# Optimization experiments

Measured on AMD Instinct MI355X. Metric: run time of the kernel, lower is better.

Reference implementation:

```python
import jax, jax.numpy as jnp
import numpy as np

HEADS = 16
DIM_HEAD = 64


def setup_inputs() -> dict:
    key = jax.random.key(0)
    k1, k2, k3, k4 = jax.random.split(key, 4)
    b, sq, skv, dim = 2, 2048, 2048, 1024
    inner = HEADS * DIM_HEAD
    return {
        "x_q": jax.random.normal(k1, (b, sq, dim), dtype=jnp.float32),
        "x_kv": jax.random.normal(k2, (b, skv, dim), dtype=jnp.float32),
        "W_qkv": jax.random.normal(k3, (dim, 3 * inner), dtype=jnp.float32) * (dim ** -0.5),
        "W_out": jax.random.normal(k4, (inner, dim), dtype=jnp.float32) * (inner ** -0.5),
        "b_out": jnp.zeros((dim,), dtype=jnp.float32),
    }


def reference(x_q, x_kv, W_qkv, W_out, b_out):
    b, sq, dim = x_q.shape
    skv = x_kv.shape[1]
    inner = HEADS * DIM_HEAD
    scale = DIM_HEAD ** -0.5
    # to_qkv on concat([x_q, x_kv], seq) as in the original (bias-free linear)
    qkv = jnp.concatenate([x_q, x_kv], axis=1) @ W_qkv  # [b, sq+skv, 3*inner]
    q, k, v = jnp.split(qkv, 3, axis=-1)
    q = q[:, :sq].reshape(b, sq, HEADS, DIM_HEAD).transpose(0, 2, 1, 3)   # [b,h,sq,d]
    k = k[:, sq:].reshape(b, skv, HEADS, DIM_HEAD).transpose(0, 2, 1, 3)  # [b,h,skv,d]
    v = v[:, sq:].reshape(b, skv, HEADS, DIM_HEAD).transpose(0, 2, 1, 3)  # [b,h,skv,d]
    dots = jnp.einsum('bhqd,bhkd->bhqk', q, k) * scale
    attn = jax.nn.softmax(dots, axis=-1)  # dropout p=0.0 -> identity
    out = jnp.einsum('bhqk,bhkd->bhqd', attn, v)
    out = out.transpose(0, 2, 1, 3).reshape(b, sq, inner)
    return out @ W_out + b_out
```

## Files before the change

### kernel.cpp

```cpp
#include <hip/hip_runtime.h>


typedef __attribute__((ext_vector_type(8))) short short8;
typedef __attribute__((ext_vector_type(4))) short short4v;
typedef __attribute__((ext_vector_type(4))) float floatx4;
typedef __attribute__((ext_vector_type(16))) float floatx16;

#define QSCALE 0.18033688f

#if __has_builtin(__builtin_amdgcn_exp2f)
#define EXP2(x) __builtin_amdgcn_exp2f(x)
#else
#define EXP2(x) exp2f(x)
#endif

__device__ __forceinline__ ushort f2b(float f) {
  union { float f; unsigned u; } x; x.f = f;
  unsigned r = (x.u + 0x7fffu + ((x.u >> 16) & 1u)) >> 16;
  return (ushort)r;
}

__device__ __forceinline__ unsigned f2b2(float a, float b) {
  union { float f; unsigned u; } x, y; x.f = a; y.f = b;
  return __builtin_amdgcn_perm(y.u + 0x8000u, x.u + 0x8000u, 0x07060302u);
}

__device__ __forceinline__ unsigned cvtpk(float a, float b) {
  unsigned r;
  asm("v_cvt_pk_bf16_f32 %0, %1, %2" : "=v"(r) : "v"(a), "v"(b));
  return r;
}

#define GLL(gp, lp)                                                            \
  __builtin_amdgcn_global_load_lds(                                            \
      (const __attribute__((address_space(1))) void*)(gp),                     \
      (__attribute__((address_space(3))) void*)(lp), 16, 0, 0)

__global__ void prep(const float* __restrict__ xq, const float* __restrict__ xkv,
                     ushort* __restrict__ oq, ushort* __restrict__ okv,
                     const float* __restrict__ Wqkv, ushort* __restrict__ WqkvT,
                     const float* __restrict__ Wout, ushort* __restrict__ WoutT) {
  __shared__ float tile[32][33];
  int bid = blockIdx.x;
  const int n = 4096 * 1024;
  if (bid < 2048) {
    bool lo = bid < 1024;
    const float* in = lo ? xq : xkv;
    ushort* out = lo ? oq : okv;
    int b2 = lo ? bid : bid - 1024;
    int stride = 1024 * 256 * 4;
    for (int i = (b2 * 256 + (int)threadIdx.x) * 4; i < n; i += stride) {
      float4 v = *(const float4*)(in + i);
      uint2 o;
      o.x = f2b2(v.x, v.y);
      o.y = f2b2(v.z, v.w);
      *(uint2*)(out + i) = o;
    }
    return;
  }
  int tb = bid - 2048;
  int bx = tb & 127, by = tb >> 7;
  bool first = bx < 96;
  const float* in = first ? Wqkv : Wout;
  ushort* out = first ? WqkvT : WoutT;
  int N = first ? 3072 : 1024;
  int bxx = first ? bx : bx - 96;
  int k0 = by * 32, n0 = bxx * 32;
  int tx = threadIdx.x & 31, ty = threadIdx.x >> 5;
#pragma unroll
  for (int i = 0; i < 32; i += 8)
    tile[ty + i][tx] = in[(size_t)(k0 + ty + i) * N + n0 + tx];
  __syncthreads();
#pragma unroll
  for (int i = 0; i < 32; i += 8)
    out[(size_t)(n0 + ty + i) * 1024 + k0 + tx] = f2b(tile[tx][ty + i]);
}

__global__ __launch_bounds__(256, 3) void gemm_qkv(
    const ushort* __restrict__ Aq, const ushort* __restrict__ Akv,
    const ushort* __restrict__ Bt,
    ushort* __restrict__ Cq, ushort* __restrict__ Ck, ushort* __restrict__ Cv) {
  __shared__ __align__(16) ushort smem[17408];
  ushort* Asb = smem;
  ushort* Bsb = smem + 8192;
  const int n0 = blockIdx.x * 128, m0 = blockIdx.y * 128;
  const ushort* A = (blockIdx.x >= 8) ? Akv : Aq;
  const int t = threadIdx.x;
  const int w = t >> 6, lane = t & 63, dl = lane & 15, g = lane >> 4;
  const int wm = (w >> 1) * 64, wn = (w & 1) * 64;
  const int K = 1024;

  auto stage = [&](int buf, int k0) {
#pragma unroll
    for (int p = 0; p < 2; p++) {
      int j = t + p * 256;
      int row = j >> 2, slot = j & 3, c = (slot - row) & 3;
      GLL(A + (size_t)(m0 + row) * K + k0 + c * 8, &Asb[buf * 4096 + j * 8]);
    }
#pragma unroll
    for (int p = 0; p < 2; p++) {
      int j = t + p * 256;
      int row = j >> 2, slot = j & 3, c = (slot - row) & 3;
      GLL(Bt + (size_t)(n0 + row) * K + k0 + c * 8, &Bsb[buf * 4096 + j * 8]);
    }
  };

  const floatx4 fz = {0.f, 0.f, 0.f, 0.f};
  floatx4 acc[4][4];
#pragma unroll
  for (int i = 0; i < 4; i++)
#pragma unroll
    for (int j = 0; j < 4; j++) acc[i][j] = fz;

  stage(0, 0);
  for (int kt = 0; kt < 32; kt++) {
    int cur = kt & 1;
    __builtin_amdgcn_s_waitcnt(0);
    __syncthreads();
    if (kt + 1 < 32) stage(cur ^ 1, (kt + 1) * 32);
    short8 af[4], bf[4];
#pragma unroll
    for (int mt = 0; mt < 4; mt++) {
      int row = wm + mt * 16 + dl;
      af[mt] = *(const short8*)&Asb[cur * 4096 + row * 32 + ((g + row) & 3) * 8];
    }
#pragma unroll
    for (int nt = 0; nt < 4; nt++) {
      int row = wn + nt * 16 + dl;
      bf[nt] = *(const short8*)&Bsb[cur * 4096 + row * 32 + ((g + row) & 3) * 8];
    }
#pragma unroll
    for (int mt = 0; mt < 4; mt++)
#pragma unroll
      for (int nt = 0; nt < 4; nt++)
        acc[mt][nt] = __builtin_amdgcn_mfma_f32_16x16x32_bf16(af[mt], bf[nt], acc[mt][nt], 0, 0, 0);
  }

  if (blockIdx.x < 16) {
#pragma unroll
    for (int mt = 0; mt < 4; mt++)
#pragma unroll
      for (int nt = 0; nt < 4; nt++) {
        int gcol = n0 + wn + nt * 16 + dl;
        int row0 = m0 + wm + mt * 16 + g * 4;
        if (gcol < 1024) {
#pragma unroll
          for (int r = 0; r < 4; r++)
            Cq[(size_t)(row0 + r) * 1024 + gcol] = f2b(acc[mt][nt][r] * QSCALE);
        } else {
#pragma unroll
          for (int r = 0; r < 4; r++)
            Ck[(size_t)(row0 + r) * 1024 + gcol - 1024] = f2b(acc[mt][nt][r]);
        }
      }
  } else {
    __syncthreads();
#pragma unroll
    for (int mt = 0; mt < 4; mt++)
#pragma unroll
      for (int nt = 0; nt < 4; nt++) {
        int ncol = wn + nt * 16 + dl;
        int mrow = wm + mt * 16 + g * 4;
        uint2 pk;
        pk.x = f2b2(acc[mt][nt][0], acc[mt][nt][1]);
        pk.y = f2b2(acc[mt][nt][2], acc[mt][nt][3]);
        *(uint2*)&smem[ncol * 136 + mrow] = pk;
      }
    __syncthreads();
    int hd0 = n0 - 2048;
    int bb = m0 >> 11;
    int kv0 = m0 & 2047;
#pragma unroll
    for (int p = 0; p < 8; p++) {
      int j = t + p * 256;
      int row = j >> 4, c = j & 15;
      short8 v = *(const short8*)&smem[row * 136 + c * 8];
      *(short8*)(Cv + ((size_t)(bb * 1024 + hd0 + row)) * 2048 + kv0 + c * 8) = v;
    }
  }
}

__global__ __launch_bounds__(256, 3) void gemm_out(
    const ushort* __restrict__ A, const ushort* __restrict__ Bt,
    float* __restrict__ C, const float* __restrict__ bias) {
  __shared__ __align__(16) ushort As[2][128 * 64];
  __shared__ __align__(16) ushort Bs[2][64 * 64];
  const int n0 = blockIdx.x * 64, m0 = blockIdx.y * 128;
  const int t = threadIdx.x;
  const int w = t >> 6, lane = t & 63, dl = lane & 15, g = lane >> 4;
  const int wm = (w >> 1) * 64, wn = (w & 1) * 32;
  const int K = 1024;

  auto stage = [&](int buf, int k0) {
#pragma unroll
    for (int p = 0; p < 4; p++) {
      int j = t + p * 256;
      int row = j >> 3, slot = j & 7, c = (slot - row) & 7;
      GLL(A + (size_t)(m0 + row) * K + k0 + c * 8, &As[buf][j * 8]);
    }
#pragma unroll
    for (int p = 0; p < 2; p++) {
      int j = t + p * 256;
      int row = j >> 3, slot = j & 7, c = (slot - row) & 7;
      GLL(Bt + (size_t)(n0 + row) * K + k0 + c * 8, &Bs[buf][j * 8]);
    }
  };

  const floatx4 fz = {0.f, 0.f, 0.f, 0.f};
  floatx4 acc[4][2];
#pragma unroll
  for (int i = 0; i < 4; i++)
#pragma unroll
    for (int j = 0; j < 2; j++) acc[i][j] = fz;

  stage(0, 0);
  for (int kt = 0; kt < 16; kt++) {
    int cur = kt & 1;
    __builtin_amdgcn_s_waitcnt(0);
    __syncthreads();
    if (kt + 1 < 16) stage(cur ^ 1, (kt + 1) * 64);
#pragma unroll
    for (int ks = 0; ks < 2; ks++) {
      short8 af[4], bf[2];
#pragma unroll
      for (int mt = 0; mt < 4; mt++) {
        int row = wm + mt * 16 + dl;
        af[mt] = *(const short8*)&As[cur][row * 64 + ((ks * 4 + g + row) & 7) * 8];
      }
#pragma unroll
      for (int nt = 0; nt < 2; nt++) {
        int row = wn + nt * 16 + dl;
        bf[nt] = *(const short8*)&Bs[cur][row * 64 + ((ks * 4 + g + row) & 7) * 8];
      }
#pragma unroll
      for (int mt = 0; mt < 4; mt++)
#pragma unroll
        for (int nt = 0; nt < 2; nt++)
          acc[mt][nt] = __builtin_amdgcn_mfma_f32_16x16x32_bf16(af[mt], bf[nt], acc[mt][nt], 0, 0, 0);
    }
  }
#pragma unroll
  for (int mt = 0; mt < 4; mt++)
#pragma unroll
    for (int nt = 0; nt < 2; nt++) {
      int gcol = n0 + wn + nt * 16 + dl;
      int row0 = m0 + wm + mt * 16 + g * 4;
      float badd = bias[gcol];
#pragma unroll
      for (int r = 0; r < 4; r++)
        C[(size_t)(row0 + r) * 1024 + gcol] = acc[mt][nt][r] + badd;
    }
}

__global__ __launch_bounds__(256, 2) void attn(
    const ushort* __restrict__ Qb,
    const ushort* __restrict__ Kb,
    const ushort* __restrict__ Vt,
    ushort* __restrict__ Ob) {
  __shared__ __align__(16) ushort Ks[2][128 * 64];
  __shared__ __align__(16) ushort Vs[2][64 * 128];

  const int bh = blockIdx.x, b = bh >> 4, h = bh & 15;
  const int q0 = blockIdx.y * 128;
  const int t = threadIdx.x, w = t >> 6, lane = t & 63;
  const int l31 = lane & 31, l5 = lane >> 5;

  const ushort* Kg = Kb + (size_t)(b * 2048) * 1024 + h * 64;
  const ushort* Vg = Vt + (size_t)(b * 1024 + h * 64) * 2048;

  short8 bq[4];
  {
    int qa = q0 + w * 32 + l31;
    const ushort* qrow = Qb + (size_t)(b * 2048 + qa) * 1024 + h * 64;
#pragma unroll
    for (int ks = 0; ks < 4; ks++)
      bq[ks] = *(const short8*)(qrow + ks * 16 + l5 * 8);
  }

  auto stageK = [&](int buf, int kv0) {
#pragma unroll
    for (int p = 0; p < 4; p++) {
      int j = t + p * 256;
      int row = j >> 3, slot = j & 7, c = (slot - row - (row >> 3)) & 7;
      GLL(Kg + (size_t)(kv0 + row) * 1024 + c * 8, &Ks[buf][j * 8]);
    }
  };
  auto stageV = [&](int buf, int kv0) {
#pragma unroll
    for (int p = 0; p < 4; p++) {
      int j = t + p * 256;
      int row = j >> 4, slot = j & 15, c = (slot - row - (row >> 3)) & 15;
      GLL(Vg + (size_t)row * 2048 + kv0 + c * 8, &Vs[buf][j * 8]);
    }
  };
  stageK(0, 0);
  stageV(0, 0);

  floatx16 o2[2];
#pragma unroll
  for (int m2 = 0; m2 < 2; m2++)
#pragma unroll
    for (int r = 0; r < 16; r++) o2[m2][r] = 0.f;
  floatx4 l4 = {0.f, 0.f, 0.f, 0.f};

  for (int it = 0; it < 16; it++) {
    int cur = it & 1;
    __builtin_amdgcn_s_waitcnt(0);
    __syncthreads();
    if (it + 1 < 16) { stageK(cur ^ 1, (it + 1) * 128); stageV(cur ^ 1, (it + 1) * 128); }

    short8 bp[8];
#pragma unroll
    for (int m2 = 0; m2 < 4; m2++) {
      floatx16 s;
#pragma unroll
      for (int r = 0; r < 16; r++) s[r] = 0.f;
      int row = m2 * 32 + l31;
      __builtin_amdgcn_s_setprio(1);
#pragma unroll
      for (int ks = 0; ks < 4; ks++) {
        short8 a = *(const short8*)
            &Ks[cur][row * 64 + ((ks * 2 + l5 + row + (row >> 3)) & 7) * 8];
        s = __builtin_amdgcn_mfma_f32_32x32x16_bf16(a, bq[ks], s, 0, 0, 0);
      }
      __builtin_amdgcn_s_setprio(0);
#pragma unroll
      for (int r = 0; r < 16; r++) s[r] = EXP2(s[r]);
#pragma unroll
      for (int r = 0; r < 16; r++) l4[r & 3] += s[r];
      unsigned pk[8];
#pragma unroll
      for (int p = 0; p < 8; p++)
        pk[p] = cvtpk(s[2 * p], s[2 * p + 1]);
#pragma unroll
      for (int hf = 0; hf < 2; hf++) {
        unsigned x0 = pk[hf * 4 + 0], y0 = pk[hf * 4 + 2];
        unsigned x1 = pk[hf * 4 + 1], y1 = pk[hf * 4 + 3];
        asm("v_permlane32_swap_b32 %0, %1" : "+v"(x0), "+v"(y0));
        asm("v_permlane32_swap_b32 %0, %1" : "+v"(x1), "+v"(y1));
        union { unsigned u[4]; short8 s8; } fu;
        fu.u[0] = x0; fu.u[1] = x1; fu.u[2] = y0; fu.u[3] = y1;
        bp[m2 * 2 + hf] = fu.s8;
      }
    }

    __builtin_amdgcn_s_setprio(1);
#pragma unroll
    for (int kt = 0; kt < 8; kt++)
#pragma unroll
      for (int m2 = 0; m2 < 2; m2++) {
        int row = m2 * 32 + l31;
        short8 av = *(const short8*)
            &Vs[cur][row * 128 + ((kt * 2 + l5 + row + (row >> 3)) & 15) * 8];
        o2[m2] = __builtin_amdgcn_mfma_f32_32x32x16_bf16(av, bp[kt], o2[m2], 0, 0, 0);
      }
    __builtin_amdgcn_s_setprio(0);
  }

  float l = (l4[0] + l4[1]) + (l4[2] + l4[3]);
  l += __shfl_xor(l, 32);
  float inv_l = 1.f / l;

  __syncthreads();
  ushort* Ot = &Ks[0][0];
  {
    int q = w * 32 + l31;
#pragma unroll
    for (int m2 = 0; m2 < 2; m2++)
#pragma unroll
      for (int pp = 0; pp < 4; pp++) {
        uint2 pk2;
        pk2.x = cvtpk(o2[m2][4 * pp + 0] * inv_l, o2[m2][4 * pp + 1] * inv_l);
        pk2.y = cvtpk(o2[m2][4 * pp + 2] * inv_l, o2[m2][4 * pp + 3] * inv_l);
        int s = m2 * 8 + 2 * pp + l5;
        *(uint2*)&Ot[q * 64 + ((s + q) & 15) * 4] = pk2;
      }
  }
  asm volatile("" ::: "memory");
#pragma unroll
  for (int p = 0; p < 4; p++) {
    int j = lane + p * 64;
    int r32 = j >> 3, c = j & 7;
    int qr = w * 32 + r32;
    short4v lo = *(const short4v*)&Ot[qr * 64 + ((2 * c + qr) & 15) * 4];
    short4v hi = *(const short4v*)&Ot[qr * 64 + ((2 * c + 1 + qr) & 15) * 4];
    short8 v = {lo.x, lo.y, lo.z, lo.w, hi.x, hi.y, hi.z, hi.w};
    *(short8*)(Ob + (size_t)(b * 2048 + q0 + qr) * 1024 + h * 64 + c * 8) = v;
  }
}

extern "C" void kernel_launch(void* const* d_in, const int* in_sizes, int n_in,
                              void* d_out, int out_size, void* d_ws, size_t ws_size,
                              hipStream_t stream) {
  const float* x_q  = (const float*)d_in[0];
  const float* x_kv = (const float*)d_in[1];
  const float* Wqkv = (const float*)d_in[2];
  const float* Wout = (const float*)d_in[3];
  const float* bout = (const float*)d_in[4];
  float* out = (float*)d_out;

  char* p = (char*)d_ws;
  ushort* Xq    = (ushort*)p; p += (size_t)4096 * 1024 * 2;
  ushort* Xkv   = (ushort*)p; p += (size_t)4096 * 1024 * 2;
  ushort* WqkvT = (ushort*)p; p += (size_t)3072 * 1024 * 2;
  ushort* WoutT = (ushort*)p; p += (size_t)1024 * 1024 * 2;
  ushort* Qb    = (ushort*)p; p += (size_t)4096 * 1024 * 2;
  ushort* Kb    = (ushort*)p; p += (size_t)4096 * 1024 * 2;
  ushort* Vt    = (ushort*)p; p += (size_t)2 * 1024 * 2048 * 2;
  ushort* Ob    = (ushort*)p; p += (size_t)4096 * 1024 * 2;

  prep<<<6144, 256, 0, stream>>>(x_q, x_kv, Xq, Xkv, Wqkv, WqkvT, Wout, WoutT);
  gemm_qkv<<<dim3(24, 32), 256, 0, stream>>>(Xq, Xkv, WqkvT, Qb, Kb, Vt);
  attn<<<dim3(32, 16), 256, 0, stream>>>(Qb, Kb, Vt, Ob);
  gemm_out<<<dim3(16, 32), 256, 0, stream>>>(Ob, WoutT, out, bout);
}
```

Before: 189.5 us.

## Split attention KV range across two wave groups per block and merge partials

The attention block grows from 256 to 512 threads. Each half of the waves processes one half of the key/value sequence in 64-wide tiles with its own double-buffered shared memory. The unnormalized partial outputs and row sums are merged through shared memory before normalization and the store. This is safe without a running max because the exponentials are never max-subtracted. The aim is more waves per CU to hide latency, at the cost of a shared-memory reduction step, extra barriers, and a simpler swizzle that may raise bank conflicts.

```diff
diff --git a/kernel.cpp b/kernel.cpp
--- a/kernel.cpp
+++ b/kernel.cpp
@@ -252,25 +252,27 @@
     }
 }
 
-__global__ __launch_bounds__(256, 2) void attn(
+__global__ __launch_bounds__(512, 4) void attn(
     const ushort* __restrict__ Qb,
     const ushort* __restrict__ Kb,
     const ushort* __restrict__ Vt,
     ushort* __restrict__ Ob) {
-  __shared__ __align__(16) ushort Ks[2][128 * 64];
-  __shared__ __align__(16) ushort Vs[2][64 * 128];
+  __shared__ __align__(16) ushort Ks[2][2][64 * 64];
+  __shared__ __align__(16) ushort Vs[2][2][64 * 64];
 
   const int bh = blockIdx.x, b = bh >> 4, h = bh & 15;
   const int q0 = blockIdx.y * 128;
   const int t = threadIdx.x, w = t >> 6, lane = t & 63;
   const int l31 = lane & 31, l5 = lane >> 5;
-
-  const ushort* Kg = Kb + (size_t)(b * 2048) * 1024 + h * 64;
-  const ushort* Vg = Vt + (size_t)(b * 1024 + h * 64) * 2048;
+  const int qw = w & 3, kvh = w >> 2;
+  const int th = t & 255;
+
+  const ushort* Kg = Kb + (size_t)(b * 2048 + kvh * 1024) * 1024 + h * 64;
+  const ushort* Vg = Vt + (size_t)(b * 1024 + h * 64) * 2048 + kvh * 1024;
 
   short8 bq[4];
   {
-    int qa = q0 + w * 32 + l31;
+    int qa = q0 + qw * 32 + l31;
     const ushort* qrow = Qb + (size_t)(b * 2048 + qa) * 1024 + h * 64;
 #pragma unroll
     for (int ks = 0; ks < 4; ks++)
@@ -279,18 +281,18 @@
 
   auto stageK = [&](int buf, int kv0) {
 #pragma unroll
-    for (int p = 0; p < 4; p++) {
-      int j = t + p * 256;
-      int row = j >> 3, slot = j & 7, c = (slot - row - (row >> 3)) & 7;
-      GLL(Kg + (size_t)(kv0 + row) * 1024 + c * 8, &Ks[buf][j * 8]);
+    for (int p = 0; p < 2; p++) {
+      int j = th + p * 256;
+      int row = j >> 3, slot = j & 7, c = (slot - row) & 7;
+      GLL(Kg + (size_t)(kv0 + row) * 1024 + c * 8, &Ks[kvh][buf][j * 8]);
     }
   };
   auto stageV = [&](int buf, int kv0) {
 #pragma unroll
-    for (int p = 0; p < 4; p++) {
-      int j = t + p * 256;
-      int row = j >> 4, slot = j & 15, c = (slot - row - (row >> 3)) & 15;
-      GLL(Vg + (size_t)row * 2048 + kv0 + c * 8, &Vs[buf][j * 8]);
+    for (int p = 0; p < 2; p++) {
+      int j = th + p * 256;
+      int row = j >> 3, slot = j & 7, c = (slot - row) & 7;
+      GLL(Vg + (size_t)row * 2048 + kv0 + c * 8, &Vs[kvh][buf][j * 8]);
     }
   };
   stageK(0, 0);
@@ -307,11 +309,11 @@
     int cur = it & 1;
     __builtin_amdgcn_s_waitcnt(0);
     __syncthreads();
-    if (it + 1 < 16) { stageK(cur ^ 1, (it + 1) * 128); stageV(cur ^ 1, (it + 1) * 128); }
-
-    short8 bp[8];
-#pragma unroll
-    for (int m2 = 0; m2 < 4; m2++) {
+    if (it + 1 < 16) { stageK(cur ^ 1, (it + 1) * 64); stageV(cur ^ 1, (it + 1) * 64); }
+
+    short8 bp[4];
+#pragma unroll
+    for (int m2 = 0; m2 < 2; m2++) {
       floatx16 s;
 #pragma unroll
       for (int r = 0; r < 16; r++) s[r] = 0.f;
@@ -320,7 +322,7 @@
 #pragma unroll
       for (int ks = 0; ks < 4; ks++) {
         short8 a = *(const short8*)
-            &Ks[cur][row * 64 + ((ks * 2 + l5 + row + (row >> 3)) & 7) * 8];
+            &Ks[kvh][cur][row * 64 + ((ks * 2 + l5 + row) & 7) * 8];
         s = __builtin_amdgcn_mfma_f32_32x32x16_bf16(a, bq[ks], s, 0, 0, 0);
       }
       __builtin_amdgcn_s_setprio(0);
@@ -346,25 +348,51 @@
 
     __builtin_amdgcn_s_setprio(1);
 #pragma unroll
-    for (int kt = 0; kt < 8; kt++)
+    for (int kt = 0; kt < 4; kt++)
 #pragma unroll
       for (int m2 = 0; m2 < 2; m2++) {
         int row = m2 * 32 + l31;
         short8 av = *(const short8*)
-            &Vs[cur][row * 128 + ((kt * 2 + l5 + row + (row >> 3)) & 15) * 8];
+            &Vs[kvh][cur][row * 64 + ((kt * 2 + l5 + row) & 7) * 8];
         o2[m2] = __builtin_amdgcn_mfma_f32_32x32x16_bf16(av, bp[kt], o2[m2], 0, 0, 0);
       }
     __builtin_amdgcn_s_setprio(0);
   }
 
-  float l = (l4[0] + l4[1]) + (l4[2] + l4[3]);
-  l += __shfl_xor(l, 32);
+  float lp = (l4[0] + l4[1]) + (l4[2] + l4[3]);
+
+  __syncthreads();
+  float2* Of = (float2*)&Ks[0][0][0];
+  float*  Lf = (float*)&Vs[0][0][0];
+  if (kvh == 1) {
+#pragma unroll
+    for (int m2 = 0; m2 < 2; m2++)
+#pragma unroll
+      for (int p = 0; p < 8; p++) {
+        float2 v = {o2[m2][2 * p], o2[m2][2 * p + 1]};
+        Of[(m2 * 8 + p) * 256 + qw * 64 + lane] = v;
+      }
+    Lf[qw * 64 + lane] = lp;
+  }
+  __syncthreads();
+  if (kvh == 0) {
+#pragma unroll
+    for (int m2 = 0; m2 < 2; m2++)
+#pragma unroll
+      for (int p = 0; p < 8; p++) {
+        float2 v = Of[(m2 * 8 + p) * 256 + qw * 64 + lane];
+        o2[m2][2 * p] += v.x;
+        o2[m2][2 * p + 1] += v.y;
+      }
+    lp += Lf[qw * 64 + lane];
+  }
+  float l = lp + __shfl_xor(lp, 32);
   float inv_l = 1.f / l;
 
   __syncthreads();
-  ushort* Ot = &Ks[0][0];
-  {
-    int q = w * 32 + l31;
+  ushort* Ot = &Ks[0][0][0];
+  if (kvh == 0) {
+    int q = qw * 32 + l31;
 #pragma unroll
     for (int m2 = 0; m2 < 2; m2++)
 #pragma unroll
@@ -377,15 +405,17 @@
       }
   }
   asm volatile("" ::: "memory");
-#pragma unroll
-  for (int p = 0; p < 4; p++) {
-    int j = lane + p * 64;
-    int r32 = j >> 3, c = j & 7;
-    int qr = w * 32 + r32;
-    short4v lo = *(const short4v*)&Ot[qr * 64 + ((2 * c + qr) & 15) * 4];
-    short4v hi = *(const short4v*)&Ot[qr * 64 + ((2 * c + 1 + qr) & 15) * 4];
-    short8 v = {lo.x, lo.y, lo.z, lo.w, hi.x, hi.y, hi.z, hi.w};
-    *(short8*)(Ob + (size_t)(b * 2048 + q0 + qr) * 1024 + h * 64 + c * 8) = v;
+  if (kvh == 0) {
+#pragma unroll
+    for (int p = 0; p < 4; p++) {
+      int j = lane + p * 64;
+      int r32 = j >> 3, c = j & 7;
+      int qr = qw * 32 + r32;
+      short4v lo = *(const short4v*)&Ot[qr * 64 + ((2 * c + qr) & 15) * 4];
+      short4v hi = *(const short4v*)&Ot[qr * 64 + ((2 * c + 1 + qr) & 15) * 4];
+      short8 v = {lo.x, lo.y, lo.z, lo.w, hi.x, hi.y, hi.z, hi.w};
+      *(short8*)(Ob + (size_t)(b * 2048 + q0 + qr) * 1024 + h * 64 + c * 8) = v;
+    }
   }
 }
 
@@ -411,6 +441,6 @@
 
   prep<<<6144, 256, 0, stream>>>(x_q, x_kv, Xq, Xkv, Wqkv, WqkvT, Wout, WoutT);
   gemm_qkv<<<dim3(24, 32), 256, 0, stream>>>(Xq, Xkv, WqkvT, Qb, Kb, Vt);
-  attn<<<dim3(32, 16), 256, 0, stream>>>(Qb, Kb, Vt, Ob);
+  attn<<<dim3(32, 16), 512, 0, stream>>>(Qb, Kb, Vt, Ob);
   gemm_out<<<dim3(16, 32), 256, 0, stream>>>(Ob, WoutT, out, bout);
 }
```

Measured after the change: 192.1 us. No clear change (+1.4%).
